# Performance work log

Hardware: AMD Instinct MI355X
Metric: run time of the kernel (lower is better)

Reference implementation:

```python
import jax, jax.numpy as jnp
import numpy as np

N_NODES = 100000
N_EDGES = 1600000
IN_DIM, HID_DIM, OUT_DIM = 256, 64, 64


def gcn_conv(x, src, dst, W, b, n_nodes):
    """PyG GCNConv: D^-1/2 (A + I) D^-1/2 X W + b (self-loops added, deg on dst)."""
    h = x @ W  # [N, D_out]
    ones = jnp.ones(src.shape[0], dtype=h.dtype)
    deg = jax.ops.segment_sum(ones, dst, num_segments=n_nodes) + 1.0  # +1 for self-loop
    dinv = jax.lax.rsqrt(deg)  # deg >= 1, always finite
    norm = dinv[src] * dinv[dst]  # [E]
    # neighbor aggregation (scatter-add) + self-loop contribution
    agg = jax.ops.segment_sum(h[src] * norm[:, None], dst, num_segments=n_nodes)
    agg = agg + h * (dinv * dinv)[:, None]
    return agg + b


def gcn_backbone(x, edge_index, W1, b1, W2, b2, n_nodes):
    src, dst = edge_index[0], edge_index[1]
    h = jax.nn.relu(gcn_conv(x, src, dst, W1, b1, n_nodes))
    h = gcn_conv(h, src, dst, W2, b2, n_nodes)
    return h


def zscore(h):
    # torch .std(0) is unbiased (ddof=1)
    return (h - h.mean(axis=0)) / jnp.std(h, axis=0, ddof=1)


def setup_inputs() -> dict:
    key = jax.random.key(0)
    k = jax.random.split(key, 8)
    x1 = jax.random.normal(k[0], (N_NODES, IN_DIM), dtype=jnp.float32)
    x2 = jax.random.normal(k[1], (N_NODES, IN_DIM), dtype=jnp.float32)
    edge_index1 = jax.random.randint(k[2], (2, N_EDGES), 0, N_NODES, dtype=jnp.int64)
    edge_index2 = jax.random.randint(k[3], (2, N_EDGES), 0, N_NODES, dtype=jnp.int64)
    W1 = jax.random.normal(k[4], (IN_DIM, HID_DIM), dtype=jnp.float32) * (1.0 / np.sqrt(IN_DIM))
    b1 = jnp.zeros((HID_DIM,), dtype=jnp.float32)
    W2 = jax.random.normal(k[5], (HID_DIM, OUT_DIM), dtype=jnp.float32) * (1.0 / np.sqrt(HID_DIM))
    b2 = jnp.zeros((OUT_DIM,), dtype=jnp.float32)
    return {"x1": x1, "edge_index1": edge_index1, "x2": x2, "edge_index2": edge_index2,
            "W1": W1, "b1": b1, "W2": W2, "b2": b2}


def reference(x1, edge_index1, x2, edge_index2, W1, b1, W2, b2):
    h1 = gcn_backbone(x1, edge_index1, W1, b1, W2, b2, N_NODES)
    h2 = gcn_backbone(x2, edge_index2, W1, b1, W2, b2, N_NODES)
    return zscore(h1), zscore(h2)
```

## Files before the change

### kernel.cpp

```cpp
#include <hip/hip_runtime.h>
#include <hip/hip_bf16.h>

#define HD 64
#define CH 8192
#define BKT_SHIFT 10
#define SRC_BITS 17
#define MAXBLK 256

typedef __attribute__((ext_vector_type(8))) short bf16x8;
typedef __attribute__((ext_vector_type(4))) float f32x4;
typedef __attribute__((ext_vector_type(4))) unsigned int u32x4;

#define WAITALL do { asm volatile("s_waitcnt vmcnt(0)" ::: "memory"); \
                     __builtin_amdgcn_sched_barrier(0); } while (0)

__device__ inline unsigned short f2bf(float x) {
  unsigned u = __float_as_uint(x);
  unsigned r = u + 0x7FFF + ((u >> 16) & 1);
  return (unsigned short)(r >> 16);
}
__device__ inline float bf2f(unsigned short h) {
  return __uint_as_float(((unsigned)h) << 16);
}

__global__ __launch_bounds__(256) void k_wprep(const float* __restrict__ W1,
                                               const float* __restrict__ W2,
                                               unsigned short* __restrict__ Wf1,
                                               unsigned short* __restrict__ Wf2hi,
                                               unsigned short* __restrict__ Wf2lo) {
  int idx = blockIdx.x * blockDim.x + threadIdx.x;
  if (idx < 256 * 64) {
    int k = idx >> 6, c = idx & 63;
    float w = W1[idx];
    int ks = k >> 5, r = k & 31, h2 = r >> 3, j = r & 7;
    int f = c >> 4, r16c = c & 15;
    int pos = (((ks * 4 + f) * 64) + h2 * 16 + r16c) * 8 + j;
    Wf1[pos] = f2bf(w);
  } else if (idx < 256 * 64 + 64 * 64) {
    int i2 = idx - 256 * 64;
    int k = i2 >> 6, c = i2 & 63;
    float w = W2[i2];
    int ks = k >> 5, r = k & 31, h2 = r >> 3, j = r & 7;
    int f = c >> 4, r16c = c & 15;
    int pos = (((ks * 4 + f) * 64) + h2 * 16 + r16c) * 8 + j;
    unsigned short hi = f2bf(w);
    Wf2hi[pos] = hi;
    Wf2lo[pos] = f2bf(w - bf2f(hi));
  }
}

__global__ __launch_bounds__(256) void k_bin1(const int* __restrict__ src0,
                                              const int* __restrict__ dst0,
                                              const int* __restrict__ src1,
                                              const int* __restrict__ dst1,
                                              int* __restrict__ tmp,
                                              int* __restrict__ counts,
                                              int* __restrict__ offsets,
                                              int NB, int NBLK, int E) {
  __shared__ int hist[128];
  __shared__ int pref[128];
  __shared__ int lofs[128];
  __shared__ int stage[CH];
  const int g = blockIdx.x / NBLK;
  const int blk = blockIdx.x % NBLK;
  const int* __restrict__ src = g ? src1 : src0;
  const int* __restrict__ dst = g ? dst1 : dst0;
  int* __restrict__ tmpg = tmp + (size_t)g * NBLK * CH;
  int* __restrict__ cntg = counts + (size_t)g * NB * NBLK;
  int* __restrict__ offg = offsets + (size_t)g * NB * NBLK;
  const int e0 = blk * CH;
  const int len = min(CH, E - e0);
  const int t = threadIdx.x;

  for (int i = t; i < 128; i += 256) hist[i] = 0;
  __syncthreads();
  int dreg[CH / 256];
#pragma unroll
  for (int it = 0; it < CH / 256; ++it) {
    int i = t + it * 256;
    if (i < len) {
      int d = dst[e0 + i];
      dreg[it] = d;
      atomicAdd(&hist[d >> BKT_SHIFT], 1);
    }
  }
  __syncthreads();
  if (t < 128) pref[t] = hist[t];
  __syncthreads();
  for (int off = 1; off < 128; off <<= 1) {
    int v = 0;
    if (t < 128 && t >= off) v = pref[t - off];
    __syncthreads();
    if (t < 128) pref[t] += v;
    __syncthreads();
  }
  if (t < NB) {
    int ex = pref[t] - hist[t];
    lofs[t] = ex;
    cntg[t * NBLK + blk] = hist[t];
    offg[t * NBLK + blk] = ex;
  }
  __syncthreads();
#pragma unroll
  for (int it = 0; it < CH / 256; ++it) {
    int i = t + it * 256;
    if (i < len) {
      int d = dreg[it], s = src[e0 + i];
      int slot = atomicAdd(&lofs[d >> BKT_SHIFT], 1);
      stage[slot] = ((d & ((1 << BKT_SHIFT) - 1)) << SRC_BITS) | s;
    }
  }
  __syncthreads();
  int nv = len >> 2;
  for (int i = t; i < nv; i += 256) ((int4*)(tmpg + e0))[i] = ((const int4*)stage)[i];
  for (int i = (nv << 2) + t; i < len; i += 256) tmpg[e0 + i] = stage[i];
}

__global__ __launch_bounds__(128) void k_bscan(const int* __restrict__ counts,
                                               int* __restrict__ bucket_base,
                                               int* __restrict__ row_start,
                                               int NB, int NBLK, int N, int E) {
  __shared__ int sh[128];
  const int g = blockIdx.x;
  const int* __restrict__ cntg = counts + (size_t)g * NB * NBLK;
  int* __restrict__ bbg = bucket_base + g * (NB + 1);
  int* __restrict__ rsg = row_start + (size_t)g * (N + 1);
  int t = threadIdx.x;
  int v = 0;
  if (t < NB) {
    const int* p = cntg + t * NBLK;
    for (int i = 0; i < NBLK; ++i) v += p[i];
  }
  sh[t] = v;
  __syncthreads();
  for (int off = 1; off < 128; off <<= 1) {
    int x = (t >= off) ? sh[t - off] : 0;
    __syncthreads();
    sh[t] += x;
    __syncthreads();
  }
  if (t < NB) bbg[t] = sh[t] - v;
  if (t == 0) {
    bbg[NB] = E;
    rsg[N] = E;
  }
}

__global__ __launch_bounds__(1024) void k_bin2m(const int* __restrict__ tmp,
                                                const int* __restrict__ counts,
                                                const int* __restrict__ offsets,
                                                const int* __restrict__ bucket_base,
                                                int* __restrict__ row_start,
                                                float* __restrict__ dinv,
                                                int* __restrict__ recs, int N, int NB,
                                                int NBLK, int E) {
  __shared__ int h[1 << BKT_SHIFT];
  __shared__ int lcur[1 << BKT_SHIFT];
  __shared__ int scnt[MAXBLK], soff[MAXBLK];
  const int g = blockIdx.x / NB;
  const int b = blockIdx.x % NB;
  const int* __restrict__ tmpg = tmp + (size_t)g * NBLK * CH;
  const int* __restrict__ cntg = counts + (size_t)g * NB * NBLK;
  const int* __restrict__ offg = offsets + (size_t)g * NB * NBLK;
  const int* __restrict__ bbg = bucket_base + g * (NB + 1);
  int* __restrict__ rsg = row_start + (size_t)g * (N + 1);
  float* __restrict__ dig = dinv + (size_t)g * N;
  int* __restrict__ recg = recs + (size_t)g * E;
  const int t = threadIdx.x;
  const int node0 = b << BKT_SHIFT;
  const int lane = t & 63, w = t >> 6;

  h[t] = 0;
  for (int i = t; i < NBLK; i += 1024) {
    scnt[i] = cntg[b * NBLK + i];
    soff[i] = offg[b * NBLK + i];
  }
  __syncthreads();
  for (int blk = w; blk < NBLK; blk += 16) {
    int cnt = scnt[blk];
    const int* p = tmpg + blk * CH + soff[blk];
    for (int j = lane; j < cnt; j += 64) atomicAdd(&h[p[j] >> SRC_BITS], 1);
  }
  __syncthreads();
  int deg = h[t];
  __syncthreads();
  for (int off = 1; off < 1024; off <<= 1) {
    int x = (t >= off) ? h[t - off] : 0;
    __syncthreads();
    h[t] += x;
    __syncthreads();
  }
  int base = bbg[b] + h[t] - deg;
  lcur[t] = base;
  int n = node0 + t;
  if (n < N) {
    rsg[n] = base;
    dig[n] = rsqrtf((float)deg + 1.0f);
  }
  __syncthreads();
  for (int blk = w; blk < NBLK; blk += 16) {
    int cnt = scnt[blk];
    const int* p = tmpg + blk * CH + soff[blk];
    for (int j = lane; j < cnt; j += 64) {
      int rec = p[j];
      int d = rec >> SRC_BITS;
      int s = rec & ((1 << SRC_BITS) - 1);
      int slot = atomicAdd(&lcur[d], 1);
      recg[slot] = s;
    }
  }
}

__global__ __launch_bounds__(256) void k_gemm1(const float* __restrict__ X0,
                                               const float* __restrict__ X1,
                                               const unsigned short* __restrict__ Wf1,
                                               unsigned short* __restrict__ Hb, int N,
                                               int gPer) {
  const int tid = threadIdx.x;
  const int g = blockIdx.x / gPer;
  const int bblk = blockIdx.x % gPer;
  const float* __restrict__ Xv = g ? X1 : X0;
  const int lane = tid & 63;
  const int wv = tid >> 6;
  const int r16 = lane & 15;
  const int half = lane >> 4;
  const int row = bblk * 64 + wv * 16 + r16;
  const int rowc = min(row, N - 1);

  unsigned long long xa =
      (unsigned long long)(const void*)(Xv + (size_t)rowc * 256 + half * 8);
  f32x4 a[16];
  asm volatile(
      "global_load_dwordx4 %0, %16, off\n\t"
      "global_load_dwordx4 %1, %16, off offset:16\n\t"
      "global_load_dwordx4 %2, %16, off offset:128\n\t"
      "global_load_dwordx4 %3, %16, off offset:144\n\t"
      "global_load_dwordx4 %4, %16, off offset:256\n\t"
      "global_load_dwordx4 %5, %16, off offset:272\n\t"
      "global_load_dwordx4 %6, %16, off offset:384\n\t"
      "global_load_dwordx4 %7, %16, off offset:400\n\t"
      "global_load_dwordx4 %8, %16, off offset:512\n\t"
      "global_load_dwordx4 %9, %16, off offset:528\n\t"
      "global_load_dwordx4 %10, %16, off offset:640\n\t"
      "global_load_dwordx4 %11, %16, off offset:656\n\t"
      "global_load_dwordx4 %12, %16, off offset:768\n\t"
      "global_load_dwordx4 %13, %16, off offset:784\n\t"
      "global_load_dwordx4 %14, %16, off offset:896\n\t"
      "global_load_dwordx4 %15, %16, off offset:912\n\t"
      : "=&v"(a[0]), "=&v"(a[1]), "=&v"(a[2]), "=&v"(a[3]), "=&v"(a[4]),
        "=&v"(a[5]), "=&v"(a[6]), "=&v"(a[7]), "=&v"(a[8]), "=&v"(a[9]),
        "=&v"(a[10]), "=&v"(a[11]), "=&v"(a[12]), "=&v"(a[13]), "=&v"(a[14]),
        "=&v"(a[15])
      : "v"(xa));

  const unsigned long long wb = (unsigned long long)(const void*)Wf1 + lane * 16;
  bf16x8 B[32];
  asm volatile(
      "global_load_dwordx4 %0, %16, off\n\t"
      "global_load_dwordx4 %1, %16, off offset:1024\n\t"
      "global_load_dwordx4 %2, %16, off offset:2048\n\t"
      "global_load_dwordx4 %3, %16, off offset:3072\n\t"
      "global_load_dwordx4 %4, %17, off\n\t"
      "global_load_dwordx4 %5, %17, off offset:1024\n\t"
      "global_load_dwordx4 %6, %17, off offset:2048\n\t"
      "global_load_dwordx4 %7, %17, off offset:3072\n\t"
      "global_load_dwordx4 %8, %18, off\n\t"
      "global_load_dwordx4 %9, %18, off offset:1024\n\t"
      "global_load_dwordx4 %10, %18, off offset:2048\n\t"
      "global_load_dwordx4 %11, %18, off offset:3072\n\t"
      "global_load_dwordx4 %12, %19, off\n\t"
      "global_load_dwordx4 %13, %19, off offset:1024\n\t"
      "global_load_dwordx4 %14, %19, off offset:2048\n\t"
      "global_load_dwordx4 %15, %19, off offset:3072\n\t"
      : "=&v"(B[0]), "=&v"(B[1]), "=&v"(B[2]), "=&v"(B[3]), "=&v"(B[4]),
        "=&v"(B[5]), "=&v"(B[6]), "=&v"(B[7]), "=&v"(B[8]), "=&v"(B[9]),
        "=&v"(B[10]), "=&v"(B[11]), "=&v"(B[12]), "=&v"(B[13]), "=&v"(B[14]),
        "=&v"(B[15])
      : "v"(wb), "v"(wb + 4096), "v"(wb + 8192), "v"(wb + 12288));

  WAITALL;

  asm volatile(
      "global_load_dwordx4 %0, %16, off\n\t"
      "global_load_dwordx4 %1, %16, off offset:1024\n\t"
      "global_load_dwordx4 %2, %16, off offset:2048\n\t"
      "global_load_dwordx4 %3, %16, off offset:3072\n\t"
      "global_load_dwordx4 %4, %17, off\n\t"
      "global_load_dwordx4 %5, %17, off offset:1024\n\t"
      "global_load_dwordx4 %6, %17, off offset:2048\n\t"
      "global_load_dwordx4 %7, %17, off offset:3072\n\t"
      "global_load_dwordx4 %8, %18, off\n\t"
      "global_load_dwordx4 %9, %18, off offset:1024\n\t"
      "global_load_dwordx4 %10, %18, off offset:2048\n\t"
      "global_load_dwordx4 %11, %18, off offset:3072\n\t"
      "global_load_dwordx4 %12, %19, off\n\t"
      "global_load_dwordx4 %13, %19, off offset:1024\n\t"
      "global_load_dwordx4 %14, %19, off offset:2048\n\t"
      "global_load_dwordx4 %15, %19, off offset:3072\n\t"
      : "=&v"(B[16]), "=&v"(B[17]), "=&v"(B[18]), "=&v"(B[19]), "=&v"(B[20]),
        "=&v"(B[21]), "=&v"(B[22]), "=&v"(B[23]), "=&v"(B[24]), "=&v"(B[25]),
        "=&v"(B[26]), "=&v"(B[27]), "=&v"(B[28]), "=&v"(B[29]), "=&v"(B[30]),
        "=&v"(B[31])
      : "v"(wb + 16384), "v"(wb + 20480), "v"(wb + 24576), "v"(wb + 28672));

  f32x4 acc[4];
#pragma unroll
  for (int f = 0; f < 4; ++f) acc[f] = (f32x4){0.f, 0.f, 0.f, 0.f};

#pragma unroll
  for (int ks = 0; ks < 4; ++ks) {
    union { __hip_bfloat162 h[4]; bf16x8 v; } cu;
    cu.h[0] = __float22bfloat162_rn(make_float2(a[2 * ks][0], a[2 * ks][1]));
    cu.h[1] = __float22bfloat162_rn(make_float2(a[2 * ks][2], a[2 * ks][3]));
    cu.h[2] = __float22bfloat162_rn(make_float2(a[2 * ks + 1][0], a[2 * ks + 1][1]));
    cu.h[3] = __float22bfloat162_rn(make_float2(a[2 * ks + 1][2], a[2 * ks + 1][3]));
#pragma unroll
    for (int f = 0; f < 4; ++f)
      acc[f] = __builtin_amdgcn_mfma_f32_16x16x32_bf16(cu.v, B[ks * 4 + f], acc[f], 0, 0, 0);
  }

  WAITALL;

#pragma unroll
  for (int ks = 4; ks < 8; ++ks) {
    union { __hip_bfloat162 h[4]; bf16x8 v; } cu;
    cu.h[0] = __float22bfloat162_rn(make_float2(a[2 * ks][0], a[2 * ks][1]));
    cu.h[1] = __float22bfloat162_rn(make_float2(a[2 * ks][2], a[2 * ks][3]));
    cu.h[2] = __float22bfloat162_rn(make_float2(a[2 * ks + 1][0], a[2 * ks + 1][1]));
    cu.h[3] = __float22bfloat162_rn(make_float2(a[2 * ks + 1][2], a[2 * ks + 1][3]));
#pragma unroll
    for (int f = 0; f < 4; ++f)
      acc[f] = __builtin_amdgcn_mfma_f32_16x16x32_bf16(cu.v, B[ks * 4 + f], acc[f], 0, 0, 0);
  }

  const int orow0 = bblk * 64 + wv * 16 + half * 4;
#pragma unroll
  for (int f = 0; f < 4; ++f) {
#pragma unroll
    for (int rg = 0; rg < 4; ++rg) {
      int orow = orow0 + rg;
      if (orow < N) Hb[((size_t)g * N + orow) * HD + f * 16 + r16] = f2bf(acc[f][rg]);
    }
  }
}

__global__ __launch_bounds__(256) void k_gemm2(const unsigned short* __restrict__ Xb,
                                               const unsigned short* __restrict__ Wfh,
                                               const unsigned short* __restrict__ Wfl,
                                               unsigned short* __restrict__ Hb, int M) {
  const int tid = threadIdx.x;
  const int row0 = blockIdx.x * 64;
  const int lane = tid & 63;
  const int wv = tid >> 6;
  const int r16 = lane & 15;
  const int half = lane >> 4;
  const int row = row0 + wv * 16 + r16;
  const int rowc = min(row, M - 1);

  unsigned long long xa =
      (unsigned long long)(const void*)(Xb + (size_t)rowc * 64 + half * 8);
  const unsigned long long bh = (unsigned long long)(const void*)Wfh + lane * 16;
  const unsigned long long bl = (unsigned long long)(const void*)Wfl + lane * 16;
  u32x4 A0, A1;
  bf16x8 BH[8], BL[8];
  asm volatile(
      "global_load_dwordx4 %0, %18, off\n\t"
      "global_load_dwordx4 %1, %18, off offset:64\n\t"
      "global_load_dwordx4 %2, %19, off\n\t"
      "global_load_dwordx4 %3, %19, off offset:1024\n\t"
      "global_load_dwordx4 %4, %19, off offset:2048\n\t"
      "global_load_dwordx4 %5, %19, off offset:3072\n\t"
      "global_load_dwordx4 %6, %20, off\n\t"
      "global_load_dwordx4 %7, %20, off offset:1024\n\t"
      "global_load_dwordx4 %8, %20, off offset:2048\n\t"
      "global_load_dwordx4 %9, %20, off offset:3072\n\t"
      "global_load_dwordx4 %10, %21, off\n\t"
      "global_load_dwordx4 %11, %21, off offset:1024\n\t"
      "global_load_dwordx4 %12, %21, off offset:2048\n\t"
      "global_load_dwordx4 %13, %21, off offset:3072\n\t"
      "global_load_dwordx4 %14, %22, off\n\t"
      "global_load_dwordx4 %15, %22, off offset:1024\n\t"
      "global_load_dwordx4 %16, %22, off offset:2048\n\t"
      "global_load_dwordx4 %17, %22, off offset:3072\n\t"
      : "=&v"(A0), "=&v"(A1), "=&v"(BH[0]), "=&v"(BH[1]), "=&v"(BH[2]),
        "=&v"(BH[3]), "=&v"(BH[4]), "=&v"(BH[5]), "=&v"(BH[6]), "=&v"(BH[7]),
        "=&v"(BL[0]), "=&v"(BL[1]), "=&v"(BL[2]), "=&v"(BL[3]), "=&v"(BL[4]),
        "=&v"(BL[5]), "=&v"(BL[6]), "=&v"(BL[7])
      : "v"(xa), "v"(bh), "v"(bh + 4096), "v"(bl), "v"(bl + 4096));

  WAITALL;

  f32x4 acc[4];
#pragma unroll
  for (int f = 0; f < 4; ++f) acc[f] = (f32x4){0.f, 0.f, 0.f, 0.f};

  union { u32x4 u; bf16x8 v; } a0u, a1u;
  a0u.u = A0;
  a1u.u = A1;
#pragma unroll
  for (int f = 0; f < 4; ++f) {
    acc[f] = __builtin_amdgcn_mfma_f32_16x16x32_bf16(a0u.v, BH[f], acc[f], 0, 0, 0);
    acc[f] = __builtin_amdgcn_mfma_f32_16x16x32_bf16(a0u.v, BL[f], acc[f], 0, 0, 0);
    acc[f] = __builtin_amdgcn_mfma_f32_16x16x32_bf16(a1u.v, BH[4 + f], acc[f], 0, 0, 0);
    acc[f] = __builtin_amdgcn_mfma_f32_16x16x32_bf16(a1u.v, BL[4 + f], acc[f], 0, 0, 0);
  }

  const int orow0 = row0 + wv * 16 + half * 4;
#pragma unroll
  for (int f = 0; f < 4; ++f) {
#pragma unroll
    for (int rg = 0; rg < 4; ++rg) {
      int orow = orow0 + rg;
      if (orow < M) Hb[(size_t)orow * HD + f * 16 + r16] = f2bf(acc[f][rg]);
    }
  }
}

template <int OUTBF16>
__global__ __launch_bounds__(256) void k_agg(const unsigned short* __restrict__ Hb,
                                             const int* __restrict__ recs,
                                             const int* __restrict__ row_start,
                                             const float* __restrict__ dinv,
                                             const float* __restrict__ bias,
                                             void* __restrict__ outv, int N, int E,
                                             int relu) {
  const int t = threadIdx.x;
  const int nglob = (blockIdx.x * blockDim.x + t) >> 4;
  const int lane16 = t & 15;
  if (nglob >= 2 * N) return;
  const int g = nglob >= N;
  const int node = nglob - g * N;
  const int* __restrict__ rsg = row_start + (size_t)g * (N + 1);
  const int* __restrict__ R = recs + (size_t)g * E;
  const float* __restrict__ dig = dinv + (size_t)g * N;
  const unsigned short* __restrict__ Hbg = Hb + (size_t)g * N * HD;

  const int c0 = lane16 * 4;
  float di = dig[node];
  float a0, a1, a2, a3;
  {
    uint2 h = *(const uint2*)&Hbg[(size_t)node * HD + c0];
    float dd = di * di;
    a0 = bf2f((unsigned short)(h.x & 0xffff)) * dd;
    a1 = bf2f((unsigned short)(h.x >> 16)) * dd;
    a2 = bf2f((unsigned short)(h.y & 0xffff)) * dd;
    a3 = bf2f((unsigned short)(h.y >> 16)) * dd;
  }
  const int beg = rsg[node], end = rsg[node + 1];
  int e = beg;
  for (; e + 8 <= end; e += 8) {
    int s[8];
    uint2 gg[8];
    float n[8];
#pragma unroll
    for (int j = 0; j < 8; ++j) s[j] = R[e + j];
#pragma unroll
    for (int j = 0; j < 8; ++j) {
      gg[j] = *(const uint2*)&Hbg[(size_t)s[j] * HD + c0];
      n[j] = dig[s[j]];
    }
#pragma unroll
    for (int j = 0; j < 8; ++j) {
      float nn = n[j] * di;
      a0 = fmaf(bf2f((unsigned short)(gg[j].x & 0xffff)), nn, a0);
      a1 = fmaf(bf2f((unsigned short)(gg[j].x >> 16)), nn, a1);
      a2 = fmaf(bf2f((unsigned short)(gg[j].y & 0xffff)), nn, a2);
      a3 = fmaf(bf2f((unsigned short)(gg[j].y >> 16)), nn, a3);
    }
  }
  for (; e < end; ++e) {
    int s = R[e];
    uint2 gg = *(const uint2*)&Hbg[(size_t)s * HD + c0];
    float nn = dig[s] * di;
    a0 = fmaf(bf2f((unsigned short)(gg.x & 0xffff)), nn, a0);
    a1 = fmaf(bf2f((unsigned short)(gg.x >> 16)), nn, a1);
    a2 = fmaf(bf2f((unsigned short)(gg.y & 0xffff)), nn, a2);
    a3 = fmaf(bf2f((unsigned short)(gg.y >> 16)), nn, a3);
  }
  float4 bv = *(const float4*)&bias[c0];
  a0 += bv.x; a1 += bv.y; a2 += bv.z; a3 += bv.w;
  if (relu) {
    a0 = fmaxf(a0, 0.f); a1 = fmaxf(a1, 0.f);
    a2 = fmaxf(a2, 0.f); a3 = fmaxf(a3, 0.f);
  }
  if (OUTBF16) {
    uint2 o;
    o.x = ((unsigned)f2bf(a1) << 16) | f2bf(a0);
    o.y = ((unsigned)f2bf(a3) << 16) | f2bf(a2);
    *(uint2*)&((unsigned short*)outv)[(size_t)nglob * HD + c0] = o;
  } else {
    *(float4*)&((float*)outv)[(size_t)nglob * HD + c0] = make_float4(a0, a1, a2, a3);
  }
}


__global__ void k_colstats(const float* __restrict__ H, float* __restrict__ stats, int N,
                           int gridPer) {
  __shared__ float ss[256], sq[256];
  const int g = blockIdx.x / gridPer;
  const int blk = blockIdx.x % gridPer;
  const float* __restrict__ Hg = H + (size_t)g * N * HD;
  float* __restrict__ st = stats + g * 128;
  int t = threadIdx.x;
  int col = t & 63, grp = t >> 6;
  float s = 0.f, q = 0.f;
  for (int row = blk * 4 + grp; row < N; row += gridPer * 4) {
    float v = Hg[(size_t)row * HD + col];
    s += v;
    q += v * v;
  }
  ss[t] = s;
  sq[t] = q;
  __syncthreads();
  if (t < 64) {
    s = ss[t] + ss[t + 64] + ss[t + 128] + ss[t + 192];
    q = sq[t] + sq[t + 64] + sq[t + 128] + sq[t + 192];
    atomicAdd(&st[t], s);
    atomicAdd(&st[64 + t], q);
  }
}

__global__ void k_normalize(float* __restrict__ H, const float* __restrict__ stats, int N) {
  int i = blockIdx.x * blockDim.x + threadIdx.x;
  int total = 2 * N * HD;
  if (i >= total) return;
  int col = i & 63;
  const float* st = stats + (i >= N * HD ? 128 : 0);
  float sum = st[col], sumsq = st[64 + col];
  float mean = sum / (float)N;
  float var = (sumsq - sum * sum / (float)N) / (float)(N - 1);
  float r = rsqrtf(var);
  H[i] = (H[i] - mean) * r;
}


extern "C" void kernel_launch(void* const* d_in, const int* in_sizes, int n_in,
                              void* d_out, int out_size, void* d_ws, size_t ws_size,
                              hipStream_t stream) {
  const int IN_DIM = 256;
  const float* X1 = (const float*)d_in[0];
  const float* X2 = (const float*)d_in[2];
  const int* EI1 = (const int*)d_in[1];
  const int* EI2 = (const int*)d_in[3];
  const float* W1 = (const float*)d_in[4];
  const float* b1 = (const float*)d_in[5];
  const float* W2 = (const float*)d_in[6];
  const float* b2 = (const float*)d_in[7];
  const int N = in_sizes[0] / IN_DIM;
  const int E = in_sizes[1] / 2;
  const int NB = (N + (1 << BKT_SHIFT) - 1) >> BKT_SHIFT;
  const int NBLK = (E + CH - 1) / CH;

  char* ws = (char*)d_ws;
  size_t off = 0;
  auto carve = [&](size_t bytes) -> char* {
    char* p = ws + off;
    off += (bytes + 255) & ~(size_t)255;
    return p;
  };
  unsigned short* Hb = (unsigned short*)carve((size_t)2 * N * HD * 2);
  int* tmp = (int*)carve((size_t)2 * NBLK * CH * 4);
  int* recs = (int*)carve((size_t)2 * E * 4);
  char* zero_base = carve(256 * 4);
  float* stats = (float*)zero_base;
  int* row_start = (int*)carve((size_t)2 * (N + 1) * 4);
  float* dinv = (float*)carve((size_t)2 * N * 4);
  int* bucket_base = (int*)carve((size_t)2 * (NB + 1) * 4);
  int* counts = (int*)carve((size_t)2 * NB * NBLK * 4);
  int* offsets = (int*)carve((size_t)2 * NB * NBLK * 4);
  unsigned short* Wf1 = (unsigned short*)carve(256 * 64 * 2);
  unsigned short* Wf2hi = (unsigned short*)carve(64 * 64 * 2);
  unsigned short* Wf2lo = (unsigned short*)carve(64 * 64 * 2);
  unsigned short* bufAgg = (unsigned short*)d_out;
  (void)ws_size; (void)n_in; (void)out_size;

  const int T = 256;
  const int gPer1 = (N + 63) / 64;
  const int gG2 = (2 * N + 63) / 64;
  const int gAgg = (2 * N * 16 + T - 1) / T;
  const int gCS = 512;
  const int gElem = (2 * N * HD + T - 1) / T;
  const int gWp = (256 * 64 + 64 * 64 + T - 1) / T;

  (void)hipMemsetAsync(zero_base, 0, 256 * 4, stream);
  k_wprep<<<gWp, T, 0, stream>>>(W1, W2, Wf1, Wf2hi, Wf2lo);
  k_bin1<<<2 * NBLK, T, 0, stream>>>(EI1, EI1 + E, EI2, EI2 + E, tmp, counts, offsets,
                                     NB, NBLK, E);
  k_bscan<<<2, 128, 0, stream>>>(counts, bucket_base, row_start, NB, NBLK, N, E);
  k_bin2m<<<2 * NB, 1024, 0, stream>>>(tmp, counts, offsets, bucket_base, row_start,
                                       dinv, recs, N, NB, NBLK, E);

  k_gemm1<<<2 * gPer1, T, 0, stream>>>(X1, X2, Wf1, Hb, N, gPer1);
  k_agg<1><<<gAgg, T, 0, stream>>>(Hb, recs, row_start, dinv, b1, bufAgg, N, E, 1);
  k_gemm2<<<gG2, T, 0, stream>>>(bufAgg, Wf2hi, Wf2lo, Hb, 2 * N);
  k_agg<0><<<gAgg, T, 0, stream>>>(Hb, recs, row_start, dinv, b2, d_out, N, E, 0);

  k_colstats<<<2 * gCS, T, 0, stream>>>((float*)d_out, stats, N, gCS);
  k_normalize<<<gElem, T, 0, stream>>>((float*)d_out, stats, N);
}
```

Baseline: 369.5 us.

## Merge layer-1 GEMM and edge binning pass into one heterogeneous kernel

```diff
diff --git a/kernel.cpp b/kernel.cpp
--- a/kernel.cpp
+++ b/kernel.cpp
@@ -49,28 +49,162 @@
   }
 }
 
-__global__ __launch_bounds__(256) void k_bin1(const int* __restrict__ src0,
-                                              const int* __restrict__ dst0,
-                                              const int* __restrict__ src1,
-                                              const int* __restrict__ dst1,
-                                              int* __restrict__ tmp,
-                                              int* __restrict__ counts,
-                                              int* __restrict__ offsets,
-                                              int NB, int NBLK, int E) {
+__global__ __launch_bounds__(256) void k_front(
+    const float* __restrict__ X0, const float* __restrict__ X1,
+    const unsigned short* __restrict__ Wf1, unsigned short* __restrict__ Hb,
+    int N, int gPer,
+    const int* __restrict__ srcA, const int* __restrict__ dstA,
+    const int* __restrict__ srcB, const int* __restrict__ dstB,
+    int* __restrict__ tmp, int* __restrict__ counts, int* __restrict__ offsets,
+    int NB, int NBLK, int E) {
   __shared__ int hist[128];
   __shared__ int pref[128];
   __shared__ int lofs[128];
   __shared__ int stage[CH];
-  const int g = blockIdx.x / NBLK;
-  const int blk = blockIdx.x % NBLK;
-  const int* __restrict__ src = g ? src1 : src0;
-  const int* __restrict__ dst = g ? dst1 : dst0;
+  const int tid = threadIdx.x;
+  const int bid = blockIdx.x;
+  const int nGemm = 2 * gPer;
+
+  if (bid < nGemm) {
+    const int g = bid / gPer;
+    const int bblk = bid % gPer;
+    const float* __restrict__ Xv = g ? X1 : X0;
+    const int lane = tid & 63;
+    const int wv = tid >> 6;
+    const int r16 = lane & 15;
+    const int half = lane >> 4;
+    const int row = bblk * 64 + wv * 16 + r16;
+    const int rowc = min(row, N - 1);
+
+    unsigned long long xa =
+        (unsigned long long)(const void*)(Xv + (size_t)rowc * 256 + half * 8);
+    f32x4 a[16];
+    asm volatile(
+        "global_load_dwordx4 %0, %16, off\n\t"
+        "global_load_dwordx4 %1, %16, off offset:16\n\t"
+        "global_load_dwordx4 %2, %16, off offset:128\n\t"
+        "global_load_dwordx4 %3, %16, off offset:144\n\t"
+        "global_load_dwordx4 %4, %16, off offset:256\n\t"
+        "global_load_dwordx4 %5, %16, off offset:272\n\t"
+        "global_load_dwordx4 %6, %16, off offset:384\n\t"
+        "global_load_dwordx4 %7, %16, off offset:400\n\t"
+        "global_load_dwordx4 %8, %16, off offset:512\n\t"
+        "global_load_dwordx4 %9, %16, off offset:528\n\t"
+        "global_load_dwordx4 %10, %16, off offset:640\n\t"
+        "global_load_dwordx4 %11, %16, off offset:656\n\t"
+        "global_load_dwordx4 %12, %16, off offset:768\n\t"
+        "global_load_dwordx4 %13, %16, off offset:784\n\t"
+        "global_load_dwordx4 %14, %16, off offset:896\n\t"
+        "global_load_dwordx4 %15, %16, off offset:912\n\t"
+        : "=&v"(a[0]), "=&v"(a[1]), "=&v"(a[2]), "=&v"(a[3]), "=&v"(a[4]),
+          "=&v"(a[5]), "=&v"(a[6]), "=&v"(a[7]), "=&v"(a[8]), "=&v"(a[9]),
+          "=&v"(a[10]), "=&v"(a[11]), "=&v"(a[12]), "=&v"(a[13]), "=&v"(a[14]),
+          "=&v"(a[15])
+        : "v"(xa));
+
+    const unsigned long long wb = (unsigned long long)(const void*)Wf1 + lane * 16;
+    bf16x8 B[32];
+    asm volatile(
+        "global_load_dwordx4 %0, %16, off\n\t"
+        "global_load_dwordx4 %1, %16, off offset:1024\n\t"
+        "global_load_dwordx4 %2, %16, off offset:2048\n\t"
+        "global_load_dwordx4 %3, %16, off offset:3072\n\t"
+        "global_load_dwordx4 %4, %17, off\n\t"
+        "global_load_dwordx4 %5, %17, off offset:1024\n\t"
+        "global_load_dwordx4 %6, %17, off offset:2048\n\t"
+        "global_load_dwordx4 %7, %17, off offset:3072\n\t"
+        "global_load_dwordx4 %8, %18, off\n\t"
+        "global_load_dwordx4 %9, %18, off offset:1024\n\t"
+        "global_load_dwordx4 %10, %18, off offset:2048\n\t"
+        "global_load_dwordx4 %11, %18, off offset:3072\n\t"
+        "global_load_dwordx4 %12, %19, off\n\t"
+        "global_load_dwordx4 %13, %19, off offset:1024\n\t"
+        "global_load_dwordx4 %14, %19, off offset:2048\n\t"
+        "global_load_dwordx4 %15, %19, off offset:3072\n\t"
+        : "=&v"(B[0]), "=&v"(B[1]), "=&v"(B[2]), "=&v"(B[3]), "=&v"(B[4]),
+          "=&v"(B[5]), "=&v"(B[6]), "=&v"(B[7]), "=&v"(B[8]), "=&v"(B[9]),
+          "=&v"(B[10]), "=&v"(B[11]), "=&v"(B[12]), "=&v"(B[13]), "=&v"(B[14]),
+          "=&v"(B[15])
+        : "v"(wb), "v"(wb + 4096), "v"(wb + 8192), "v"(wb + 12288));
+
+    WAITALL;
+
+    asm volatile(
+        "global_load_dwordx4 %0, %16, off\n\t"
+        "global_load_dwordx4 %1, %16, off offset:1024\n\t"
+        "global_load_dwordx4 %2, %16, off offset:2048\n\t"
+        "global_load_dwordx4 %3, %16, off offset:3072\n\t"
+        "global_load_dwordx4 %4, %17, off\n\t"
+        "global_load_dwordx4 %5, %17, off offset:1024\n\t"
+        "global_load_dwordx4 %6, %17, off offset:2048\n\t"
+        "global_load_dwordx4 %7, %17, off offset:3072\n\t"
+        "global_load_dwordx4 %8, %18, off\n\t"
+        "global_load_dwordx4 %9, %18, off offset:1024\n\t"
+        "global_load_dwordx4 %10, %18, off offset:2048\n\t"
+        "global_load_dwordx4 %11, %18, off offset:3072\n\t"
+        "global_load_dwordx4 %12, %19, off\n\t"
+        "global_load_dwordx4 %13, %19, off offset:1024\n\t"
+        "global_load_dwordx4 %14, %19, off offset:2048\n\t"
+        "global_load_dwordx4 %15, %19, off offset:3072\n\t"
+        : "=&v"(B[16]), "=&v"(B[17]), "=&v"(B[18]), "=&v"(B[19]), "=&v"(B[20]),
+          "=&v"(B[21]), "=&v"(B[22]), "=&v"(B[23]), "=&v"(B[24]), "=&v"(B[25]),
+          "=&v"(B[26]), "=&v"(B[27]), "=&v"(B[28]), "=&v"(B[29]), "=&v"(B[30]),
+          "=&v"(B[31])
+        : "v"(wb + 16384), "v"(wb + 20480), "v"(wb + 24576), "v"(wb + 28672));
+
+    f32x4 acc[4];
+#pragma unroll
+    for (int f = 0; f < 4; ++f) acc[f] = (f32x4){0.f, 0.f, 0.f, 0.f};
+
+#pragma unroll
+    for (int ks = 0; ks < 4; ++ks) {
+      union { __hip_bfloat162 h[4]; bf16x8 v; } cu;
+      cu.h[0] = __float22bfloat162_rn(make_float2(a[2 * ks][0], a[2 * ks][1]));
+      cu.h[1] = __float22bfloat162_rn(make_float2(a[2 * ks][2], a[2 * ks][3]));
+      cu.h[2] = __float22bfloat162_rn(make_float2(a[2 * ks + 1][0], a[2 * ks + 1][1]));
+      cu.h[3] = __float22bfloat162_rn(make_float2(a[2 * ks + 1][2], a[2 * ks + 1][3]));
+#pragma unroll
+      for (int f = 0; f < 4; ++f)
+        acc[f] = __builtin_amdgcn_mfma_f32_16x16x32_bf16(cu.v, B[ks * 4 + f], acc[f], 0, 0, 0);
+    }
+
+    WAITALL;
+
+#pragma unroll
+    for (int ks = 4; ks < 8; ++ks) {
+      union { __hip_bfloat162 h[4]; bf16x8 v; } cu;
+      cu.h[0] = __float22bfloat162_rn(make_float2(a[2 * ks][0], a[2 * ks][1]));
+      cu.h[1] = __float22bfloat162_rn(make_float2(a[2 * ks][2], a[2 * ks][3]));
+      cu.h[2] = __float22bfloat162_rn(make_float2(a[2 * ks + 1][0], a[2 * ks + 1][1]));
+      cu.h[3] = __float22bfloat162_rn(make_float2(a[2 * ks + 1][2], a[2 * ks + 1][3]));
+#pragma unroll
+      for (int f = 0; f < 4; ++f)
+        acc[f] = __builtin_amdgcn_mfma_f32_16x16x32_bf16(cu.v, B[ks * 4 + f], acc[f], 0, 0, 0);
+    }
+
+    const int orow0 = bblk * 64 + wv * 16 + half * 4;
+#pragma unroll
+    for (int f = 0; f < 4; ++f) {
+#pragma unroll
+      for (int rg = 0; rg < 4; ++rg) {
+        int orow = orow0 + rg;
+        if (orow < N) Hb[((size_t)g * N + orow) * HD + f * 16 + r16] = f2bf(acc[f][rg]);
+      }
+    }
+    return;
+  }
+
+  const int blk2 = bid - nGemm;
+  const int g = blk2 / NBLK;
+  const int blk = blk2 % NBLK;
+  const int* __restrict__ src = g ? srcB : srcA;
+  const int* __restrict__ dst = g ? dstB : dstA;
   int* __restrict__ tmpg = tmp + (size_t)g * NBLK * CH;
   int* __restrict__ cntg = counts + (size_t)g * NB * NBLK;
   int* __restrict__ offg = offsets + (size_t)g * NB * NBLK;
   const int e0 = blk * CH;
   const int len = min(CH, E - e0);
-  const int t = threadIdx.x;
+  const int t = tid;
 
   for (int i = t; i < 128; i += 256) hist[i] = 0;
   __syncthreads();
@@ -207,139 +341,6 @@
       int s = rec & ((1 << SRC_BITS) - 1);
       int slot = atomicAdd(&lcur[d], 1);
       recg[slot] = s;
-    }
-  }
-}
-
-__global__ __launch_bounds__(256) void k_gemm1(const float* __restrict__ X0,
-                                               const float* __restrict__ X1,
-                                               const unsigned short* __restrict__ Wf1,
-                                               unsigned short* __restrict__ Hb, int N,
-                                               int gPer) {
-  const int tid = threadIdx.x;
-  const int g = blockIdx.x / gPer;
-  const int bblk = blockIdx.x % gPer;
-  const float* __restrict__ Xv = g ? X1 : X0;
-  const int lane = tid & 63;
-  const int wv = tid >> 6;
-  const int r16 = lane & 15;
-  const int half = lane >> 4;
-  const int row = bblk * 64 + wv * 16 + r16;
-  const int rowc = min(row, N - 1);
-
-  unsigned long long xa =
-      (unsigned long long)(const void*)(Xv + (size_t)rowc * 256 + half * 8);
-  f32x4 a[16];
-  asm volatile(
-      "global_load_dwordx4 %0, %16, off\n\t"
-      "global_load_dwordx4 %1, %16, off offset:16\n\t"
-      "global_load_dwordx4 %2, %16, off offset:128\n\t"
-      "global_load_dwordx4 %3, %16, off offset:144\n\t"
-      "global_load_dwordx4 %4, %16, off offset:256\n\t"
-      "global_load_dwordx4 %5, %16, off offset:272\n\t"
-      "global_load_dwordx4 %6, %16, off offset:384\n\t"
-      "global_load_dwordx4 %7, %16, off offset:400\n\t"
-      "global_load_dwordx4 %8, %16, off offset:512\n\t"
-      "global_load_dwordx4 %9, %16, off offset:528\n\t"
-      "global_load_dwordx4 %10, %16, off offset:640\n\t"
-      "global_load_dwordx4 %11, %16, off offset:656\n\t"
-      "global_load_dwordx4 %12, %16, off offset:768\n\t"
-      "global_load_dwordx4 %13, %16, off offset:784\n\t"
-      "global_load_dwordx4 %14, %16, off offset:896\n\t"
-      "global_load_dwordx4 %15, %16, off offset:912\n\t"
-      : "=&v"(a[0]), "=&v"(a[1]), "=&v"(a[2]), "=&v"(a[3]), "=&v"(a[4]),
-        "=&v"(a[5]), "=&v"(a[6]), "=&v"(a[7]), "=&v"(a[8]), "=&v"(a[9]),
-        "=&v"(a[10]), "=&v"(a[11]), "=&v"(a[12]), "=&v"(a[13]), "=&v"(a[14]),
-        "=&v"(a[15])
-      : "v"(xa));
-
-  const unsigned long long wb = (unsigned long long)(const void*)Wf1 + lane * 16;
-  bf16x8 B[32];
-  asm volatile(
-      "global_load_dwordx4 %0, %16, off\n\t"
-      "global_load_dwordx4 %1, %16, off offset:1024\n\t"
-      "global_load_dwordx4 %2, %16, off offset:2048\n\t"
-      "global_load_dwordx4 %3, %16, off offset:3072\n\t"
-      "global_load_dwordx4 %4, %17, off\n\t"
-      "global_load_dwordx4 %5, %17, off offset:1024\n\t"
-      "global_load_dwordx4 %6, %17, off offset:2048\n\t"
-      "global_load_dwordx4 %7, %17, off offset:3072\n\t"
-      "global_load_dwordx4 %8, %18, off\n\t"
-      "global_load_dwordx4 %9, %18, off offset:1024\n\t"
-      "global_load_dwordx4 %10, %18, off offset:2048\n\t"
-      "global_load_dwordx4 %11, %18, off offset:3072\n\t"
-      "global_load_dwordx4 %12, %19, off\n\t"
-      "global_load_dwordx4 %13, %19, off offset:1024\n\t"
-      "global_load_dwordx4 %14, %19, off offset:2048\n\t"
-      "global_load_dwordx4 %15, %19, off offset:3072\n\t"
-      : "=&v"(B[0]), "=&v"(B[1]), "=&v"(B[2]), "=&v"(B[3]), "=&v"(B[4]),
-        "=&v"(B[5]), "=&v"(B[6]), "=&v"(B[7]), "=&v"(B[8]), "=&v"(B[9]),
-        "=&v"(B[10]), "=&v"(B[11]), "=&v"(B[12]), "=&v"(B[13]), "=&v"(B[14]),
-        "=&v"(B[15])
-      : "v"(wb), "v"(wb + 4096), "v"(wb + 8192), "v"(wb + 12288));
-
-  WAITALL;
-
-  asm volatile(
-      "global_load_dwordx4 %0, %16, off\n\t"
-      "global_load_dwordx4 %1, %16, off offset:1024\n\t"
-      "global_load_dwordx4 %2, %16, off offset:2048\n\t"
-      "global_load_dwordx4 %3, %16, off offset:3072\n\t"
-      "global_load_dwordx4 %4, %17, off\n\t"
-      "global_load_dwordx4 %5, %17, off offset:1024\n\t"
-      "global_load_dwordx4 %6, %17, off offset:2048\n\t"
-      "global_load_dwordx4 %7, %17, off offset:3072\n\t"
-      "global_load_dwordx4 %8, %18, off\n\t"
-      "global_load_dwordx4 %9, %18, off offset:1024\n\t"
-      "global_load_dwordx4 %10, %18, off offset:2048\n\t"
-      "global_load_dwordx4 %11, %18, off offset:3072\n\t"
-      "global_load_dwordx4 %12, %19, off\n\t"
-      "global_load_dwordx4 %13, %19, off offset:1024\n\t"
-      "global_load_dwordx4 %14, %19, off offset:2048\n\t"
-      "global_load_dwordx4 %15, %19, off offset:3072\n\t"
-      : "=&v"(B[16]), "=&v"(B[17]), "=&v"(B[18]), "=&v"(B[19]), "=&v"(B[20]),
-        "=&v"(B[21]), "=&v"(B[22]), "=&v"(B[23]), "=&v"(B[24]), "=&v"(B[25]),
-        "=&v"(B[26]), "=&v"(B[27]), "=&v"(B[28]), "=&v"(B[29]), "=&v"(B[30]),
-        "=&v"(B[31])
-      : "v"(wb + 16384), "v"(wb + 20480), "v"(wb + 24576), "v"(wb + 28672));
-
-  f32x4 acc[4];
-#pragma unroll
-  for (int f = 0; f < 4; ++f) acc[f] = (f32x4){0.f, 0.f, 0.f, 0.f};
-
-#pragma unroll
-  for (int ks = 0; ks < 4; ++ks) {
-    union { __hip_bfloat162 h[4]; bf16x8 v; } cu;
-    cu.h[0] = __float22bfloat162_rn(make_float2(a[2 * ks][0], a[2 * ks][1]));
-    cu.h[1] = __float22bfloat162_rn(make_float2(a[2 * ks][2], a[2 * ks][3]));
-    cu.h[2] = __float22bfloat162_rn(make_float2(a[2 * ks + 1][0], a[2 * ks + 1][1]));
-    cu.h[3] = __float22bfloat162_rn(make_float2(a[2 * ks + 1][2], a[2 * ks + 1][3]));
-#pragma unroll
-    for (int f = 0; f < 4; ++f)
-      acc[f] = __builtin_amdgcn_mfma_f32_16x16x32_bf16(cu.v, B[ks * 4 + f], acc[f], 0, 0, 0);
-  }
-
-  WAITALL;
-
-#pragma unroll
-  for (int ks = 4; ks < 8; ++ks) {
-    union { __hip_bfloat162 h[4]; bf16x8 v; } cu;
-    cu.h[0] = __float22bfloat162_rn(make_float2(a[2 * ks][0], a[2 * ks][1]));
-    cu.h[1] = __float22bfloat162_rn(make_float2(a[2 * ks][2], a[2 * ks][3]));
-    cu.h[2] = __float22bfloat162_rn(make_float2(a[2 * ks + 1][0], a[2 * ks + 1][1]));
-    cu.h[3] = __float22bfloat162_rn(make_float2(a[2 * ks + 1][2], a[2 * ks + 1][3]));
-#pragma unroll
-    for (int f = 0; f < 4; ++f)
-      acc[f] = __builtin_amdgcn_mfma_f32_16x16x32_bf16(cu.v, B[ks * 4 + f], acc[f], 0, 0, 0);
-  }
-
-  const int orow0 = bblk * 64 + wv * 16 + half * 4;
-#pragma unroll
-  for (int f = 0; f < 4; ++f) {
-#pragma unroll
-    for (int rg = 0; rg < 4; ++rg) {
-      int orow = orow0 + rg;
-      if (orow < N) Hb[((size_t)g * N + orow) * HD + f * 16 + r16] = f2bf(acc[f][rg]);
     }
   }
 }
@@ -584,13 +585,13 @@
 
   (void)hipMemsetAsync(zero_base, 0, 256 * 4, stream);
   k_wprep<<<gWp, T, 0, stream>>>(W1, W2, Wf1, Wf2hi, Wf2lo);
-  k_bin1<<<2 * NBLK, T, 0, stream>>>(EI1, EI1 + E, EI2, EI2 + E, tmp, counts, offsets,
-                                     NB, NBLK, E);
+  k_front<<<2 * gPer1 + 2 * NBLK, T, 0, stream>>>(X1, X2, Wf1, Hb, N, gPer1,
+                                                  EI1, EI1 + E, EI2, EI2 + E,
+                                                  tmp, counts, offsets, NB, NBLK, E);
   k_bscan<<<2, 128, 0, stream>>>(counts, bucket_base, row_start, NB, NBLK, N, E);
   k_bin2m<<<2 * NB, 1024, 0, stream>>>(tmp, counts, offsets, bucket_base, row_start,
                                        dinv, recs, N, NB, NBLK, E);
 
-  k_gemm1<<<2 * gPer1, T, 0, stream>>>(X1, X2, Wf1, Hb, N, gPer1);
   k_agg<1><<<gAgg, T, 0, stream>>>(Hb, recs, row_start, dinv, b1, bufAgg, N, E, 1);
   k_gemm2<<<gG2, T, 0, stream>>>(bufAgg, Wf2hi, Wf2lo, Hb, 2 * N);
   k_agg<0><<<gAgg, T, 0, stream>>>(Hb, recs, row_start, dinv, b2, d_out, N, E, 0);
```

Measured after the change: 364.3 us, median of 2. Within noise of the previous version (-1.4%).
